# Performance work log

Hardware: AMD Instinct MI355X
Metric: run time of the kernel (lower is better)

Reference implementation:

```python
import jax, jax.numpy as jnp
import numpy as np

N_NODES = 50000
N_EDGES = 800000
D = 128
N_GRAPHS = 64
N_CLASSES = 10


def setup_inputs() -> dict:
    key = jax.random.key(0)
    ks = jax.random.split(key, 10)
    x = jax.random.normal(ks[0], (N_NODES, D), dtype=jnp.float32)
    edge_index = jax.random.randint(ks[1], (2, N_EDGES), 0, N_NODES, dtype=jnp.int64)
    batch = jnp.sort(jax.random.randint(ks[2], (N_NODES,), 0, N_GRAPHS, dtype=jnp.int64))
    s = 1.0 / np.sqrt(D)
    W1a = jax.random.uniform(ks[3], (D, D), jnp.float32, -s, s)
    W1b = jax.random.uniform(ks[4], (D, D), jnp.float32, -s, s)
    W2a = jax.random.uniform(ks[5], (D, D), jnp.float32, -s, s)
    W2b = jax.random.uniform(ks[6], (D, D), jnp.float32, -s, s)
    Wfc = jax.random.uniform(ks[7], (D, N_CLASSES), jnp.float32, -s, s)
    return {
        "x": x, "edge_index": edge_index, "batch": batch,
        "W1a": W1a, "b1a": jnp.zeros((D,), jnp.float32),
        "W1b": W1b, "b1b": jnp.zeros((D,), jnp.float32),
        "W2a": W2a, "b2a": jnp.zeros((D,), jnp.float32),
        "W2b": W2b, "b2b": jnp.zeros((D,), jnp.float32),
        "Wfc": Wfc, "bfc": jnp.zeros((N_CLASSES,), jnp.float32),
    }


def _gin_conv(x, src, dst, Wa, ba, Wb, bb):
    # sum aggregation of neighbor messages x[src] into dst (eps = 0)
    agg = jax.ops.segment_sum(x[src], dst, num_segments=N_NODES)
    h = x + agg  # (1 + eps) * x + sum_{j->i} x_j
    h = jax.nn.relu(h @ Wa + ba)
    h = jax.nn.relu(h @ Wb + bb)
    return h


def reference(x, edge_index, batch, W1a, b1a, W1b, b1b, W2a, b2a, W2b, b2b, Wfc, bfc):
    src, dst = edge_index[0], edge_index[1]
    h = _gin_conv(x, src, dst, W1a, b1a, W1b, b1b)
    h = _gin_conv(h, src, dst, W2a, b2a, W2b, b2b)
    # global mean pool over graphs
    sums = jax.ops.segment_sum(h, batch, num_segments=N_GRAPHS)
    counts = jax.ops.segment_sum(jnp.ones((h.shape[0], 1), h.dtype), batch, num_segments=N_GRAPHS)
    pooled = sums / jnp.maximum(counts, 1.0)
    logits = pooled @ Wfc + bfc
    return jax.nn.sigmoid(logits)
```

## Files before the change

### kernel.cpp

```cpp
#include <hip/hip_runtime.h>

#define NN 50000
#define NE 800000
#define DF 128
#define NG 64
#define NC 10
#define NBK 391
#define PART_CHUNK 2048
#define PART_GRID 391
#define ACAP 3072
#define FINE_CAP 3072
#define RT 136
#define CAST_GRID 6250
#define PREP_GRID (CAST_GRID + 32)
#define POOL_GRID 391

typedef short bf16x8 __attribute__((ext_vector_type(8)));
typedef float f32x4  __attribute__((ext_vector_type(4)));

__device__ __forceinline__ void atomAddF(float* p, float v) {
  __hip_atomic_fetch_add(p, v, __ATOMIC_RELAXED, __HIP_MEMORY_SCOPE_AGENT);
}
__device__ __forceinline__ float b2f(unsigned short u) {
  union { unsigned int i; float f; } v; v.i = (unsigned int)u << 16; return v.f;
}
__device__ __forceinline__ unsigned int f2b(float f) {
  unsigned int i = __float_as_uint(f);
  return (i + 0x7fffu + ((i >> 16) & 1u)) >> 16;
}

__global__ __launch_bounds__(256) void k_prep_part(const float* __restrict__ x,
                                                   unsigned short* __restrict__ xb,
                                                   const float* __restrict__ W0,
                                                   const float* __restrict__ W1,
                                                   const float* __restrict__ W2,
                                                   const float* __restrict__ W3,
                                                   unsigned short* __restrict__ Wt,
                                                   const int* __restrict__ src,
                                                   const int* __restrict__ dst,
                                                   int* __restrict__ cnt_b,
                                                   unsigned int* __restrict__ arena)
{
  __shared__ unsigned int stage[PART_CHUNK];
  __shared__ int lhist[512], lcnt[512], lcur[512], gbase[512];
  __shared__ int pscan[256];
  const int tid = threadIdx.x;
  const int b   = blockIdx.x;

  if (b < CAST_GRID) {
    const int i = b * 256 + tid;
    const float4 v = reinterpret_cast<const float4*>(x)[i];
    uint2 o;
    o.x = f2b(v.x) | (f2b(v.y) << 16);
    o.y = f2b(v.z) | (f2b(v.w) << 16);
    reinterpret_cast<uint2*>(xb)[i] = o;
    return;
  }
  if (b < PREP_GRID) {
    const int o = (b - CAST_GRID) * 256 + tid;
    const int mat = o >> 11;
    const float* W = (mat == 0) ? W0 : (mat == 1) ? W1 : (mat == 2) ? W2 : W3;
    const int rem = o & 2047;
    const int kb = rem >> 7, n = rem & 127;
    unsigned int u[8];
#pragma unroll
    for (int j = 0; j < 8; ++j) u[j] = f2b(W[(size_t)(kb * 8 + j) * DF + n]);
    uint4 p;
    p.x = u[0] | (u[1] << 16);
    p.y = u[2] | (u[3] << 16);
    p.z = u[4] | (u[5] << 16);
    p.w = u[6] | (u[7] << 16);
    *reinterpret_cast<uint4*>(Wt + (size_t)mat * DF * DF + (size_t)rem * 8) = p;
    return;
  }

  const int vb = b - PREP_GRID;
  const int e0 = vb * PART_CHUNK;
  const int nE = min(PART_CHUNK, NE - e0);

  for (int i = tid; i < 512; i += 256) lhist[i] = 0;
  __syncthreads();
  unsigned int pk[8]; int bk[8];
#pragma unroll
  for (int i = 0; i < 8; ++i) {
    const int e = e0 + i * 256 + tid;
    if (e < NE) {
      const int d = dst[e], s = src[e];
      const int bb = d >> 7;
      bk[i] = bb;
      pk[i] = ((unsigned int)bb << 23) | ((unsigned int)(d & 127) << 16) | (unsigned int)s;
      atomicAdd(&lhist[bb], 1);
    } else bk[i] = -1;
  }
  __syncthreads();
  for (int i = tid; i < 512; i += 256) lcnt[i] = lhist[i];
  __syncthreads();
  const int s0 = lhist[2 * tid];
  const int s1 = lhist[2 * tid + 1];
  pscan[tid] = s0 + s1;
  __syncthreads();
  for (int off = 1; off < 256; off <<= 1) {
    int u = (tid >= off) ? pscan[tid - off] : 0;
    __syncthreads();
    pscan[tid] += u;
    __syncthreads();
  }
  const int ep = pscan[tid] - s0 - s1;
  __syncthreads();
  lhist[2 * tid]     = ep;
  lhist[2 * tid + 1] = ep + s0;
  lcur[2 * tid]      = ep;
  lcur[2 * tid + 1]  = ep + s0;
  __syncthreads();
#pragma unroll
  for (int i = 0; i < 8; ++i)
    if (bk[i] >= 0) {
      const int pos = atomicAdd(&lcur[bk[i]], 1);
      stage[pos] = pk[i];
    }
  __syncthreads();
  for (int i = tid; i < 512; i += 256) {
    if (i < NBK) {
      const int c = lcnt[i];
      if (c > 0) gbase[i] = atomicAdd(&cnt_b[i], c);
    }
  }
  __syncthreads();
  for (int idx = tid; idx < nE; idx += 256) {
    const unsigned int p = stage[idx];
    const int bb = (int)(p >> 23);
    arena[(size_t)bb * ACAP + gbase[bb] + (idx - lhist[bb])] = p;
  }
}

__global__ __launch_bounds__(256) void k_fine(const unsigned int* __restrict__ arena,
                                              const int* __restrict__ cnt_b,
                                              int* __restrict__ rs,
                                              unsigned short* __restrict__ es)
{
  __shared__ unsigned short les[FINE_CAP];
  __shared__ int bins[1024];
  __shared__ int partials[256];
  __shared__ int basebuf[512];
  __shared__ int bpair[256];
  const int tid = threadIdx.x;
  const int b   = blockIdx.x;

  if (b == 0 && tid == 0) rs[NN] = NE;

  for (int i = tid; i < 512; i += 256) basebuf[i] = (i < NBK) ? cnt_b[i] : 0;
  __syncthreads();
  const int t0 = basebuf[2 * tid];
  const int t1 = basebuf[2 * tid + 1];
  bpair[tid] = t0 + t1;
  __syncthreads();
  for (int off = 1; off < 256; off <<= 1) {
    int u = (tid >= off) ? bpair[tid - off] : 0;
    __syncthreads();
    bpair[tid] += u;
    __syncthreads();
  }
  const int eb = bpair[tid] - t0 - t1;
  __syncthreads();
  basebuf[2 * tid]     = eb;
  basebuf[2 * tid + 1] = eb + t0;
  __syncthreads();
  const int wbase = basebuf[b];
  const int cnt   = cnt_b[b];
  const int nbase = b << 7;
  const int nwin  = min(128, NN - nbase);
  const unsigned int* ap = arena + (size_t)b * ACAP;

  for (int i = tid; i < 1024; i += 256) bins[i] = 0;
  __syncthreads();
  for (int idx = tid; idx < cnt; idx += 256) {
    const unsigned int p = ap[idx];
    const int key = (int)(((p >> 16) & 127) << 3) | (int)((p & 0xffffu) >> 13);
    atomicAdd(&bins[key], 1);
  }
  __syncthreads();
  const int b4 = tid * 4;
  int sum = bins[b4] + bins[b4 + 1] + bins[b4 + 2] + bins[b4 + 3];
  partials[tid] = sum;
  __syncthreads();
  for (int off = 1; off < 256; off <<= 1) {
    int u = (tid >= off) ? partials[tid - off] : 0;
    __syncthreads();
    partials[tid] += u;
    __syncthreads();
  }
  int run = partials[tid] - sum;
#pragma unroll
  for (int k = 0; k < 4; ++k) {
    const int v = bins[b4 + k];
    bins[b4 + k] = run;
    run += v;
  }
  __syncthreads();
  for (int i = tid; i < nwin; i += 256) rs[nbase + i] = wbase + bins[i << 3];
  __syncthreads();
  if (cnt <= FINE_CAP) {
    for (int idx = tid; idx < cnt; idx += 256) {
      const unsigned int p = ap[idx];
      const int key = (int)(((p >> 16) & 127) << 3) | (int)((p & 0xffffu) >> 13);
      const int pos = atomicAdd(&bins[key], 1);
      les[pos] = (unsigned short)(p & 0xffffu);
    }
    __syncthreads();
    for (int i = tid; i < cnt; i += 256) es[wbase + i] = les[i];
  } else {
    for (int idx = tid; idx < cnt; idx += 256) {
      const unsigned int p = ap[idx];
      const int key = (int)(((p >> 16) & 127) << 3) | (int)((p & 0xffffu) >> 13);
      const int pos = atomicAdd(&bins[key], 1);
      es[wbase + pos] = (unsigned short)(p & 0xffffu);
    }
  }
}

__global__ __launch_bounds__(256) void k_gather(const unsigned short* __restrict__ feat,
                                                unsigned short* __restrict__ outp,
                                                const int* __restrict__ rs,
                                                const unsigned short* __restrict__ es)
{
  const int wid  = (blockIdx.x * 256 + threadIdx.x) >> 6;
  const int lane = threadIdx.x & 63;
  if (wid >= NN) return;
  const int q   = lane >> 4;
  const int l16 = lane & 15;
  const int off = l16 * 8;
  const int beg = rs[wid];
  const int end = rs[wid + 1];

  float a0 = 0.f, a1 = 0.f, a2 = 0.f, a3 = 0.f;
  float a4 = 0.f, a5 = 0.f, a6 = 0.f, a7 = 0.f;
  if (q == 0) {
    const uint4 u = *reinterpret_cast<const uint4*>(feat + (size_t)wid * DF + off);
    a0 = b2f(u.x & 0xffff); a1 = b2f(u.x >> 16);
    a2 = b2f(u.y & 0xffff); a3 = b2f(u.y >> 16);
    a4 = b2f(u.z & 0xffff); a5 = b2f(u.z >> 16);
    a6 = b2f(u.w & 0xffff); a7 = b2f(u.w >> 16);
  }

  int j = beg;
  for (; j + 15 < end; j += 16) {
    const int i0 = es[j + q];
    const int i1 = es[j + 4 + q];
    const int i2 = es[j + 8 + q];
    const int i3 = es[j + 12 + q];
    const uint4 u0 = *reinterpret_cast<const uint4*>(feat + (size_t)i0 * DF + off);
    const uint4 u1 = *reinterpret_cast<const uint4*>(feat + (size_t)i1 * DF + off);
    const uint4 u2 = *reinterpret_cast<const uint4*>(feat + (size_t)i2 * DF + off);
    const uint4 u3 = *reinterpret_cast<const uint4*>(feat + (size_t)i3 * DF + off);
    a0 += b2f(u0.x & 0xffff) + b2f(u1.x & 0xffff) + b2f(u2.x & 0xffff) + b2f(u3.x & 0xffff);
    a1 += b2f(u0.x >> 16)    + b2f(u1.x >> 16)    + b2f(u2.x >> 16)    + b2f(u3.x >> 16);
    a2 += b2f(u0.y & 0xffff) + b2f(u1.y & 0xffff) + b2f(u2.y & 0xffff) + b2f(u3.y & 0xffff);
    a3 += b2f(u0.y >> 16)    + b2f(u1.y >> 16)    + b2f(u2.y >> 16)    + b2f(u3.y >> 16);
    a4 += b2f(u0.z & 0xffff) + b2f(u1.z & 0xffff) + b2f(u2.z & 0xffff) + b2f(u3.z & 0xffff);
    a5 += b2f(u0.z >> 16)    + b2f(u1.z >> 16)    + b2f(u2.z >> 16)    + b2f(u3.z >> 16);
    a6 += b2f(u0.w & 0xffff) + b2f(u1.w & 0xffff) + b2f(u2.w & 0xffff) + b2f(u3.w & 0xffff);
    a7 += b2f(u0.w >> 16)    + b2f(u1.w >> 16)    + b2f(u2.w >> 16)    + b2f(u3.w >> 16);
  }
  for (; j + 3 < end; j += 4) {
    const int i = es[j + q];
    const uint4 u = *reinterpret_cast<const uint4*>(feat + (size_t)i * DF + off);
    a0 += b2f(u.x & 0xffff); a1 += b2f(u.x >> 16);
    a2 += b2f(u.y & 0xffff); a3 += b2f(u.y >> 16);
    a4 += b2f(u.z & 0xffff); a5 += b2f(u.z >> 16);
    a6 += b2f(u.w & 0xffff); a7 += b2f(u.w >> 16);
  }
  if (j + q < end) {
    const int i = es[j + q];
    const uint4 u = *reinterpret_cast<const uint4*>(feat + (size_t)i * DF + off);
    a0 += b2f(u.x & 0xffff); a1 += b2f(u.x >> 16);
    a2 += b2f(u.y & 0xffff); a3 += b2f(u.y >> 16);
    a4 += b2f(u.z & 0xffff); a5 += b2f(u.z >> 16);
    a6 += b2f(u.w & 0xffff); a7 += b2f(u.w >> 16);
  }

  a0 += __shfl_xor(a0, 16); a1 += __shfl_xor(a1, 16);
  a2 += __shfl_xor(a2, 16); a3 += __shfl_xor(a3, 16);
  a4 += __shfl_xor(a4, 16); a5 += __shfl_xor(a5, 16);
  a6 += __shfl_xor(a6, 16); a7 += __shfl_xor(a7, 16);
  a0 += __shfl_xor(a0, 32); a1 += __shfl_xor(a1, 32);
  a2 += __shfl_xor(a2, 32); a3 += __shfl_xor(a3, 32);
  a4 += __shfl_xor(a4, 32); a5 += __shfl_xor(a5, 32);
  a6 += __shfl_xor(a6, 32); a7 += __shfl_xor(a7, 32);

  if (q == 0) {
    uint4 o;
    o.x = f2b(a0) | (f2b(a1) << 16);
    o.y = f2b(a2) | (f2b(a3) << 16);
    o.z = f2b(a4) | (f2b(a5) << 16);
    o.w = f2b(a6) | (f2b(a7) << 16);
    *reinterpret_cast<uint4*>(outp + (size_t)wid * DF + off) = o;
  }
}

__global__ __launch_bounds__(256, 4) void k_gemm2(const unsigned short* __restrict__ Ab,
                                                  const unsigned short* __restrict__ Wta,
                                                  const float* __restrict__ ba,
                                                  const unsigned short* __restrict__ Wtb,
                                                  const float* __restrict__ bb,
                                                  unsigned short* __restrict__ outb, int M)
{
  __shared__ unsigned short hL[4][16 * RT];
  const int tid  = threadIdx.x;
  const int lane = tid & 63;
  const int w    = tid >> 6;
  const int col  = lane & 15;
  const int kq   = lane >> 4;

  const int m   = blockIdx.x * 64 + w * 16 + col;
  const int mld = (m < M) ? m : (M - 1);

  bf16x8 bc[4];
#pragma unroll
  for (int s = 0; s < 4; ++s)
    bc[s] = *reinterpret_cast<const bf16x8*>(Ab + (size_t)mld * DF + s * 32 + kq * 8);

  f32x4 acc[8];
#pragma unroll
  for (int nf = 0; nf < 8; ++nf) acc[nf] = (f32x4){0.f, 0.f, 0.f, 0.f};
#pragma unroll
  for (int s = 0; s < 4; ++s) {
#pragma unroll
    for (int nf = 0; nf < 8; ++nf) {
      const bf16x8 wa = *reinterpret_cast<const bf16x8*>(
          Wta + ((size_t)(s * 4 + kq) * 128 + nf * 16 + col) * 8);
      acc[nf] = __builtin_amdgcn_mfma_f32_16x16x32_bf16(wa, bc[s], acc[nf], 0, 0, 0);
    }
  }

  unsigned short* hw = &hL[w][0];
#pragma unroll
  for (int nf = 0; nf < 8; ++nf) {
    const float4 bva = *reinterpret_cast<const float4*>(ba + nf * 16 + kq * 4);
    uint2 pk;
    pk.x = f2b(fmaxf(acc[nf][0] + bva.x, 0.f)) | (f2b(fmaxf(acc[nf][1] + bva.y, 0.f)) << 16);
    pk.y = f2b(fmaxf(acc[nf][2] + bva.z, 0.f)) | (f2b(fmaxf(acc[nf][3] + bva.w, 0.f)) << 16);
    *reinterpret_cast<uint2*>(&hw[col * RT + nf * 16 + kq * 4]) = pk;
  }

  f32x4 acc2[8];
#pragma unroll
  for (int nf = 0; nf < 8; ++nf) acc2[nf] = (f32x4){0.f, 0.f, 0.f, 0.f};
#pragma unroll
  for (int s = 0; s < 4; ++s) {
    const bf16x8 hb = *reinterpret_cast<const bf16x8*>(&hw[col * RT + s * 32 + kq * 8]);
#pragma unroll
    for (int nf = 0; nf < 8; ++nf) {
      const bf16x8 wb = *reinterpret_cast<const bf16x8*>(
          Wtb + ((size_t)(s * 4 + kq) * 128 + nf * 16 + col) * 8);
      acc2[nf] = __builtin_amdgcn_mfma_f32_16x16x32_bf16(wb, hb, acc2[nf], 0, 0, 0);
    }
  }
  if (m < M) {
#pragma unroll
    for (int nf = 0; nf < 8; ++nf) {
      const float4 bvb = *reinterpret_cast<const float4*>(bb + nf * 16 + kq * 4);
      ushort4 p;
      p.x = (unsigned short)f2b(fmaxf(acc2[nf][0] + bvb.x, 0.f));
      p.y = (unsigned short)f2b(fmaxf(acc2[nf][1] + bvb.y, 0.f));
      p.z = (unsigned short)f2b(fmaxf(acc2[nf][2] + bvb.z, 0.f));
      p.w = (unsigned short)f2b(fmaxf(acc2[nf][3] + bvb.w, 0.f));
      *reinterpret_cast<ushort4*>(outb + (size_t)m * DF + nf * 16 + kq * 4) = p;
    }
  }
}

__global__ __launch_bounds__(256) void k_pool(const unsigned short* __restrict__ h,
                                              const int* __restrict__ batch,
                                              float* __restrict__ sums,
                                              int* __restrict__ cnts)
{
  const int wv   = (blockIdx.x * 256 + threadIdx.x) >> 6;
  const int lane = threadIdx.x & 63;
  const int n0 = wv * 32;
  if (n0 >= NN) return;
  const int n1 = min(n0 + 32, NN);
  const int off = lane * 2;

  const int gfirst = batch[n0];
  const int glast  = batch[n1 - 1];
  float ax = 0.f, ay = 0.f;

  if (gfirst == glast) {
#pragma unroll 4
    for (int i = n0; i < n1; ++i) {
      const unsigned int u = *reinterpret_cast<const unsigned int*>(h + (size_t)i * DF + off);
      ax += b2f(u & 0xffff); ay += b2f(u >> 16);
    }
    atomAddF(&sums[gfirst * DF + off],     ax);
    atomAddF(&sums[gfirst * DF + off + 1], ay);
    if (lane == 0) atomicAdd(&cnts[gfirst], n1 - n0);
  } else {
    int g = gfirst, cnt = 0;
    for (int i = n0; i < n1; ++i) {
      const int gi = batch[i];
      if (gi != g) {
        atomAddF(&sums[g * DF + off],     ax);
        atomAddF(&sums[g * DF + off + 1], ay);
        if (lane == 0) atomicAdd(&cnts[g], cnt);
        ax = 0.f; ay = 0.f; cnt = 0; g = gi;
      }
      const unsigned int u = *reinterpret_cast<const unsigned int*>(h + (size_t)i * DF + off);
      ax += b2f(u & 0xffff); ay += b2f(u >> 16);
      ++cnt;
    }
    atomAddF(&sums[g * DF + off],     ax);
    atomAddF(&sums[g * DF + off + 1], ay);
    if (lane == 0) atomicAdd(&cnts[g], cnt);
  }
}

__global__ __launch_bounds__(256) void k_head(const float* __restrict__ sums,
                                              const int* __restrict__ cnts,
                                              const float* __restrict__ Wfc,
                                              const float* __restrict__ bfc,
                                              float* __restrict__ out)
{
  const int o = blockIdx.x * 256 + threadIdx.x;
  if (o >= NG * NC) return;
  const int g = o / NC, c = o % NC;
  const float inv = 1.f / fmaxf((float)cnts[g], 1.f);
  float z = bfc[c];
#pragma unroll 8
  for (int k = 0; k < DF; ++k)
    z = fmaf(sums[g * DF + k] * inv, Wfc[k * NC + c], z);
  out[o] = 1.f / (1.f + expf(-z));
}

extern "C" void kernel_launch(void* const* d_in, const int* in_sizes, int n_in,
                              void* d_out, int out_size, void* d_ws, size_t ws_size,
                              hipStream_t stream)
{
  const float* x   = (const float*)d_in[0];
  const int*   ei  = (const int*)d_in[1];
  const int* batch = (const int*)d_in[2];
  const float* W1a = (const float*)d_in[3];
  const float* b1a = (const float*)d_in[4];
  const float* W1b = (const float*)d_in[5];
  const float* b1b = (const float*)d_in[6];
  const float* W2a = (const float*)d_in[7];
  const float* b2a = (const float*)d_in[8];
  const float* W2b = (const float*)d_in[9];
  const float* b2b = (const float*)d_in[10];
  const float* Wfc = (const float*)d_in[11];
  const float* bfc = (const float*)d_in[12];
  float* out = (float*)d_out;

  const int* src = ei;
  const int* dst = ei + NE;

  unsigned short* xb = (unsigned short*)d_ws;
  unsigned short* A  = xb + (size_t)NN * DF;
  unsigned short* H  = A + (size_t)NN * DF;
  unsigned short* Wt = H + (size_t)NN * DF;
  float* sums  = (float*)(Wt + (size_t)4 * DF * DF);
  int*   cnts  = (int*)(sums + NG * DF);
  int*   cnt_b = cnts + 64;
  int*   rs    = cnt_b + 512;
  unsigned short* es = (unsigned short*)(rs + (NN + 4));
  unsigned int* arena = (unsigned int*)(es + NE);

  unsigned short* Wt1a = Wt;
  unsigned short* Wt1b = Wt + DF * DF;
  unsigned short* Wt2a = Wt + 2 * DF * DF;
  unsigned short* Wt2b = Wt + 3 * DF * DF;

  const int gemm_grid   = (NN + 63) / 64;
  const int gather_grid = (NN * 64 + 255) / 256;

  hipMemsetAsync(sums, 0, (size_t)(NG * DF + 64 + 512) * sizeof(float), stream);
  k_prep_part<<<PREP_GRID + PART_GRID, 256, 0, stream>>>(
      x, xb, W1a, W1b, W2a, W2b, Wt, src, dst, cnt_b, arena);
  k_fine<<<NBK, 256, 0, stream>>>(arena, cnt_b, rs, es);

  k_gather<<<gather_grid, 256, 0, stream>>>(xb, A, rs, es);
  k_gemm2<<<gemm_grid, 256, 0, stream>>>(A, Wt1a, b1a, Wt1b, b1b, A, NN);

  k_gather<<<gather_grid, 256, 0, stream>>>(A, H, rs, es);
  k_gemm2<<<gemm_grid, 256, 0, stream>>>(H, Wt2a, b2a, Wt2b, b2b, H, NN);

  k_pool<<<POOL_GRID, 256, 0, stream>>>(H, batch, sums, cnts);
  k_head<<<(NG * NC + 255) / 256, 256, 0, stream>>>(sums, cnts, Wfc, bfc, out);
}
```

Measured before the change: 172.8 us.

## Fuse global mean pooling into second GIN layer GEMM epilogue

The second layer's MLP kernel now reduces its fp32 outputs straight into per-graph sums: it uses wave shuffles when all 16 rows of a tile share one graph, and per-row atomics otherwise. This removes writing the second layer's output to memory and the separate pooling kernel that read it back. Per-graph node counts are now found in the head kernel by binary search over the sorted batch array, which drops the count atomics. The workspace shrinks by reusing the xb buffer for the second gather. In exchange the epilogue issues many more atomics per tile, and pooling now sums fp32 values rather than bf16-rounded ones.

Result: slower. 194.6 us (+12.6%).

```diff
diff --git a/kernel.cpp b/kernel.cpp
--- a/kernel.cpp
+++ b/kernel.cpp
@@ -13,7 +13,6 @@
 #define RT 136
 #define CAST_GRID 6250
 #define PREP_GRID (CAST_GRID + 32)
-#define POOL_GRID 391
 
 typedef short bf16x8 __attribute__((ext_vector_type(8)));
 typedef float f32x4  __attribute__((ext_vector_type(4)));
@@ -369,53 +368,118 @@
   }
 }
 
-__global__ __launch_bounds__(256) void k_pool(const unsigned short* __restrict__ h,
+__global__ __launch_bounds__(256, 4) void k_gemm2p(const unsigned short* __restrict__ Ab,
+                                                   const unsigned short* __restrict__ Wta,
+                                                   const float* __restrict__ ba,
+                                                   const unsigned short* __restrict__ Wtb,
+                                                   const float* __restrict__ bb,
+                                                   const int* __restrict__ batch,
+                                                   float* __restrict__ sums)
+{
+  __shared__ unsigned short hL[4][16 * RT];
+  const int tid  = threadIdx.x;
+  const int lane = tid & 63;
+  const int w    = tid >> 6;
+  const int col  = lane & 15;
+  const int kq   = lane >> 4;
+
+  const int base_m = blockIdx.x * 64 + w * 16;
+  const int m   = base_m + col;
+  const int mld = (m < NN) ? m : (NN - 1);
+
+  bf16x8 bc[4];
+#pragma unroll
+  for (int s = 0; s < 4; ++s)
+    bc[s] = *reinterpret_cast<const bf16x8*>(Ab + (size_t)mld * DF + s * 32 + kq * 8);
+
+  f32x4 acc[8];
+#pragma unroll
+  for (int nf = 0; nf < 8; ++nf) acc[nf] = (f32x4){0.f, 0.f, 0.f, 0.f};
+#pragma unroll
+  for (int s = 0; s < 4; ++s) {
+#pragma unroll
+    for (int nf = 0; nf < 8; ++nf) {
+      const bf16x8 wa = *reinterpret_cast<const bf16x8*>(
+          Wta + ((size_t)(s * 4 + kq) * 128 + nf * 16 + col) * 8);
+      acc[nf] = __builtin_amdgcn_mfma_f32_16x16x32_bf16(wa, bc[s], acc[nf], 0, 0, 0);
+    }
+  }
+
+  unsigned short* hw = &hL[w][0];
+#pragma unroll
+  for (int nf = 0; nf < 8; ++nf) {
+    const float4 bva = *reinterpret_cast<const float4*>(ba + nf * 16 + kq * 4);
+    uint2 pk;
+    pk.x = f2b(fmaxf(acc[nf][0] + bva.x, 0.f)) | (f2b(fmaxf(acc[nf][1] + bva.y, 0.f)) << 16);
+    pk.y = f2b(fmaxf(acc[nf][2] + bva.z, 0.f)) | (f2b(fmaxf(acc[nf][3] + bva.w, 0.f)) << 16);
+    *reinterpret_cast<uint2*>(&hw[col * RT + nf * 16 + kq * 4]) = pk;
+  }
+
+  f32x4 acc2[8];
+#pragma unroll
+  for (int nf = 0; nf < 8; ++nf) acc2[nf] = (f32x4){0.f, 0.f, 0.f, 0.f};
+#pragma unroll
+  for (int s = 0; s < 4; ++s) {
+    const bf16x8 hb = *reinterpret_cast<const bf16x8*>(&hw[col * RT + s * 32 + kq * 8]);
+#pragma unroll
+    for (int nf = 0; nf < 8; ++nf) {
+      const bf16x8 wb = *reinterpret_cast<const bf16x8*>(
+          Wtb + ((size_t)(s * 4 + kq) * 128 + nf * 16 + col) * 8);
+      acc2[nf] = __builtin_amdgcn_mfma_f32_16x16x32_bf16(wb, hb, acc2[nf], 0, 0, 0);
+    }
+  }
+
+  if (base_m >= NN) return;
+
+#pragma unroll
+  for (int nf = 0; nf < 8; ++nf) {
+    const float4 bvb = *reinterpret_cast<const float4*>(bb + nf * 16 + kq * 4);
+    acc2[nf][0] = fmaxf(acc2[nf][0] + bvb.x, 0.f);
+    acc2[nf][1] = fmaxf(acc2[nf][1] + bvb.y, 0.f);
+    acc2[nf][2] = fmaxf(acc2[nf][2] + bvb.z, 0.f);
+    acc2[nf][3] = fmaxf(acc2[nf][3] + bvb.w, 0.f);
+  }
+
+  const int mend = min(base_m + 16, NN);
+  const int gfirst = batch[base_m];
+  const int glast  = batch[mend - 1];
+
+  if (gfirst == glast && mend == base_m + 16) {
+#pragma unroll
+    for (int nf = 0; nf < 8; ++nf) {
+#pragma unroll
+      for (int j = 0; j < 4; ++j) {
+        float v = acc2[nf][j];
+        v += __shfl_xor(v, 1);
+        v += __shfl_xor(v, 2);
+        v += __shfl_xor(v, 4);
+        v += __shfl_xor(v, 8);
+        acc2[nf][j] = v;
+      }
+    }
+    if (col == 0) {
+#pragma unroll
+      for (int nf = 0; nf < 8; ++nf) {
+#pragma unroll
+        for (int j = 0; j < 4; ++j)
+          atomAddF(&sums[gfirst * DF + nf * 16 + kq * 4 + j], acc2[nf][j]);
+      }
+    }
+  } else {
+    if (m < NN) {
+      const int g = batch[m];
+#pragma unroll
+      for (int nf = 0; nf < 8; ++nf) {
+#pragma unroll
+        for (int j = 0; j < 4; ++j)
+          atomAddF(&sums[g * DF + nf * 16 + kq * 4 + j], acc2[nf][j]);
+      }
+    }
+  }
+}
+
+__global__ __launch_bounds__(256) void k_head(const float* __restrict__ sums,
                                               const int* __restrict__ batch,
-                                              float* __restrict__ sums,
-                                              int* __restrict__ cnts)
-{
-  const int wv   = (blockIdx.x * 256 + threadIdx.x) >> 6;
-  const int lane = threadIdx.x & 63;
-  const int n0 = wv * 32;
-  if (n0 >= NN) return;
-  const int n1 = min(n0 + 32, NN);
-  const int off = lane * 2;
-
-  const int gfirst = batch[n0];
-  const int glast  = batch[n1 - 1];
-  float ax = 0.f, ay = 0.f;
-
-  if (gfirst == glast) {
-#pragma unroll 4
-    for (int i = n0; i < n1; ++i) {
-      const unsigned int u = *reinterpret_cast<const unsigned int*>(h + (size_t)i * DF + off);
-      ax += b2f(u & 0xffff); ay += b2f(u >> 16);
-    }
-    atomAddF(&sums[gfirst * DF + off],     ax);
-    atomAddF(&sums[gfirst * DF + off + 1], ay);
-    if (lane == 0) atomicAdd(&cnts[gfirst], n1 - n0);
-  } else {
-    int g = gfirst, cnt = 0;
-    for (int i = n0; i < n1; ++i) {
-      const int gi = batch[i];
-      if (gi != g) {
-        atomAddF(&sums[g * DF + off],     ax);
-        atomAddF(&sums[g * DF + off + 1], ay);
-        if (lane == 0) atomicAdd(&cnts[g], cnt);
-        ax = 0.f; ay = 0.f; cnt = 0; g = gi;
-      }
-      const unsigned int u = *reinterpret_cast<const unsigned int*>(h + (size_t)i * DF + off);
-      ax += b2f(u & 0xffff); ay += b2f(u >> 16);
-      ++cnt;
-    }
-    atomAddF(&sums[g * DF + off],     ax);
-    atomAddF(&sums[g * DF + off + 1], ay);
-    if (lane == 0) atomicAdd(&cnts[g], cnt);
-  }
-}
-
-__global__ __launch_bounds__(256) void k_head(const float* __restrict__ sums,
-                                              const int* __restrict__ cnts,
                                               const float* __restrict__ Wfc,
                                               const float* __restrict__ bfc,
                                               float* __restrict__ out)
@@ -423,7 +487,11 @@
   const int o = blockIdx.x * 256 + threadIdx.x;
   if (o >= NG * NC) return;
   const int g = o / NC, c = o % NC;
-  const float inv = 1.f / fmaxf((float)cnts[g], 1.f);
+  int lo = 0, hi = NN;
+  while (lo < hi) { const int mid = (lo + hi) >> 1; if (batch[mid] < g) lo = mid + 1; else hi = mid; }
+  int lo2 = lo, hi2 = NN;
+  while (lo2 < hi2) { const int mid = (lo2 + hi2) >> 1; if (batch[mid] < g + 1) lo2 = mid + 1; else hi2 = mid; }
+  const float inv = 1.f / fmaxf((float)(lo2 - lo), 1.f);
   float z = bfc[c];
 #pragma unroll 8
   for (int k = 0; k < DF; ++k)
@@ -455,11 +523,9 @@
 
   unsigned short* xb = (unsigned short*)d_ws;
   unsigned short* A  = xb + (size_t)NN * DF;
-  unsigned short* H  = A + (size_t)NN * DF;
-  unsigned short* Wt = H + (size_t)NN * DF;
+  unsigned short* Wt = A + (size_t)NN * DF;
   float* sums  = (float*)(Wt + (size_t)4 * DF * DF);
-  int*   cnts  = (int*)(sums + NG * DF);
-  int*   cnt_b = cnts + 64;
+  int*   cnt_b = (int*)(sums + NG * DF);
   int*   rs    = cnt_b + 512;
   unsigned short* es = (unsigned short*)(rs + (NN + 4));
   unsigned int* arena = (unsigned int*)(es + NE);
@@ -472,7 +538,7 @@
   const int gemm_grid   = (NN + 63) / 64;
   const int gather_grid = (NN * 64 + 255) / 256;
 
-  hipMemsetAsync(sums, 0, (size_t)(NG * DF + 64 + 512) * sizeof(float), stream);
+  hipMemsetAsync(sums, 0, (size_t)(NG * DF + 512) * sizeof(float), stream);
   k_prep_part<<<PREP_GRID + PART_GRID, 256, 0, stream>>>(
       x, xb, W1a, W1b, W2a, W2b, Wt, src, dst, cnt_b, arena);
   k_fine<<<NBK, 256, 0, stream>>>(arena, cnt_b, rs, es);
@@ -480,9 +546,8 @@
   k_gather<<<gather_grid, 256, 0, stream>>>(xb, A, rs, es);
   k_gemm2<<<gemm_grid, 256, 0, stream>>>(A, Wt1a, b1a, Wt1b, b1b, A, NN);
 
-  k_gather<<<gather_grid, 256, 0, stream>>>(A, H, rs, es);
-  k_gemm2<<<gemm_grid, 256, 0, stream>>>(H, Wt2a, b2a, Wt2b, b2b, H, NN);
-
-  k_pool<<<POOL_GRID, 256, 0, stream>>>(H, batch, sums, cnts);
-  k_head<<<(NG * NC + 255) / 256, 256, 0, stream>>>(sums, cnts, Wfc, bfc, out);
-}
+  k_gather<<<gather_grid, 256, 0, stream>>>(A, xb, rs, es);
+  k_gemm2p<<<gemm_grid, 256, 0, stream>>>(xb, Wt2a, b2a, Wt2b, b2b, batch, sums);
+
+  k_head<<<(NG * NC + 255) / 256, 256, 0, stream>>>(sums, batch, Wfc, bfc, out);
+}
```
